# Performance work log

Measured on AMD Instinct MI355X. Metric: run time of the kernel, lower is better.

Reference implementation:

```python
import jax, jax.numpy as jnp
import numpy as np

N_NODES = 100000
N_EDGES = 1600000
IN_CH = 64
HID = 64


def setup_inputs() -> dict:
    key = jax.random.key(0)
    ks = jax.random.split(key, 7)
    x = jax.random.normal(ks[0], (N_NODES, IN_CH), dtype=jnp.float32)
    edge_index = jax.random.randint(ks[1], (2, N_EDGES), 0, N_NODES, dtype=jnp.int64)
    node_pair = jax.random.randint(ks[2], (2,), 0, N_NODES, dtype=jnp.int64)
    W1 = jax.random.normal(ks[3], (IN_CH, HID), dtype=jnp.float32) / np.float32(np.sqrt(IN_CH))
    b1 = jnp.zeros((HID,), dtype=jnp.float32)
    W2 = jax.random.normal(ks[4], (HID, HID), dtype=jnp.float32) / np.float32(np.sqrt(HID))
    b2 = jnp.zeros((HID,), dtype=jnp.float32)
    fc_W = jax.random.normal(ks[5], (2 * HID, 1), dtype=jnp.float32) / np.float32(np.sqrt(2 * HID))
    fc_b = jnp.zeros((1,), dtype=jnp.float32)
    return {"x": x, "edge_index": edge_index, "node_pair": node_pair,
            "W1": W1, "b1": b1, "W2": W2, "b2": b2, "fc_W": fc_W, "fc_b": fc_b}


def gcn_conv(x, W, b, src, dst, n):
    # linear transform then symmetric-normalized scatter-add with self-loops (PyG GCNConv)
    h = x @ W                                   # [n, out]
    loop = jnp.arange(n, dtype=src.dtype)
    s = jnp.concatenate([src, loop])            # [E+n]
    d = jnp.concatenate([dst, loop])
    deg = jax.ops.segment_sum(jnp.ones_like(d, dtype=h.dtype), d, num_segments=n)
    dinv = jnp.where(deg > 0, jax.lax.rsqrt(deg), 0.0)
    norm = dinv[s] * dinv[d]                    # [E+n]
    out = jax.ops.segment_sum(h[s] * norm[:, None], d, num_segments=n)
    return out + b


def reference(x, edge_index, node_pair, W1, b1, W2, b2, fc_W, fc_b):
    src, dst = edge_index[0], edge_index[1]
    n = x.shape[0]
    h = jax.nn.relu(gcn_conv(x, W1, b1, src, dst, n))
    h = jax.nn.relu(gcn_conv(h, W2, b2, src, dst, n))
    z = jnp.concatenate([h[node_pair[0]], h[node_pair[1]]], axis=0)  # [2*HID]
    return jax.nn.sigmoid(z @ fc_W + fc_b)      # [1]
```

## Files before the change

kernel.cpp:

```cpp
#include <hip/hip_runtime.h>
#include <math.h>


#define CH 64
#define E1CAP 4096
#define F1CAP (E1CAP + 2)
#define E2CAP 131072
#define GRID 256
#define BLK 512
#define NWAVE (BLK / 64)
#define NP5 8
#define BMCAP 3200
#define SPIN_MAX (1 << 20)

struct Params {
    const float* x;
    const int* src; const int* dst; const int* np_;
    const float* W1; const float* b1;
    const float* W2; const float* b2;
    const float* fcW; const float* fcb;
    int* bar;
    int* ctrl;
    int* deg;
    unsigned* bmF1; unsigned* bmNd;
    int* pos1; long long* e1sd; int* F1;
    long long* e2sd; float* h1; float* agg1e;
    float* out;
    int E; int N; int bmN;
};

__device__ __forceinline__ float dinv_of(int degv) {
    return rsqrtf((float)(degv + 1));
}

__device__ __forceinline__ void st_agent(int* p, int v) {
    __hip_atomic_store(p, v, __ATOMIC_RELAXED, __HIP_MEMORY_SCOPE_AGENT);
}
__device__ __forceinline__ void st_agent_f(float* p, float v) {
    __hip_atomic_store(p, v, __ATOMIC_RELAXED, __HIP_MEMORY_SCOPE_AGENT);
}
__device__ __forceinline__ void st_agent64(long long* p, long long v) {
    __hip_atomic_store(p, v, __ATOMIC_RELAXED, __HIP_MEMORY_SCOPE_AGENT);
}
__device__ __forceinline__ int ld_agent(const int* p) {
    return __hip_atomic_load((int*)p, __ATOMIC_RELAXED, __HIP_MEMORY_SCOPE_AGENT);
}
__device__ __forceinline__ long long ld_agent64(const long long* p) {
    return __hip_atomic_load((long long*)p, __ATOMIC_RELAXED, __HIP_MEMORY_SCOPE_AGENT);
}
__device__ __forceinline__ float ld_agent_f(const float* p) {
    return __hip_atomic_load((float*)p, __ATOMIC_RELAXED, __HIP_MEMORY_SCOPE_AGENT);
}

__device__ __forceinline__ void gbar_arrive(int* bar, int phase) {
    __syncthreads();
    if (threadIdx.x == 0) {
        asm volatile("" ::: "memory");
        st_agent(&bar[blockIdx.x << 4], phase);
    }
}
__device__ __forceinline__ void gbar_wait(int* bar, int phase) {
    if (threadIdx.x < 64) {
        const int l = threadIdx.x;
        for (int it = 0; ; ++it) {
            int a = ld_agent(&bar[l << 4]);
            int b = ld_agent(&bar[(l + 64) << 4]);
            int c = ld_agent(&bar[(l + 128) << 4]);
            int d = ld_agent(&bar[(l + 192) << 4]);
            if (__all(min(min(a, b), min(c, d)) >= phase) || it > SPIN_MAX) break;
            __builtin_amdgcn_s_sleep(1);
        }
    }
    __syncthreads();
}
__device__ __forceinline__ void gbar(int* bar, int phase) {
    gbar_arrive(bar, phase);
    gbar_wait(bar, phase);
}

__device__ __forceinline__ void reg_node(int u, unsigned* bmF1, unsigned* bmNd,
                                         int* ctrl, int* F1, int* pos1) {
    unsigned bit = 1u << (u & 31);
    unsigned old = atomicOr(&bmF1[u >> 5], bit);
    if (!(old & bit)) {
        atomicOr(&bmNd[u >> 5], bit);
        int i = atomicAdd(&ctrl[2], 1);
        st_agent(&F1[i], u);
        st_agent(&pos1[u], i);
    }
}

__device__ __forceinline__ long long pack_sd(int s, int d) {
    return ((long long)(unsigned)d << 32) | (unsigned)s;
}

__device__ __forceinline__ void phase_e1f1(int gid, int gsz,
                                           const int* __restrict__ src,
                                           const int* __restrict__ dst, int E,
                                           int p0, int p1, int* ctrl,
                                           long long* e1sd,
                                           unsigned* bmF1, unsigned* bmNd,
                                           int* F1, int* pos1) {
    if (gid == 0) {
        reg_node(p0, bmF1, bmNd, ctrl, F1, pos1);
        if (p1 != p0) reg_node(p1, bmF1, bmNd, ctrl, F1, pos1);
    }
    const int nvec = E >> 2;
    const int4* dst4 = (const int4*)dst;
    for (int base = gid; base < nvec; base += gsz * 4) {
        int4 v[4];
#pragma unroll
        for (int t = 0; t < 4; t++) {
            int i = base + t * gsz;
            if (i < nvec) v[t] = dst4[i];
        }
#pragma unroll
        for (int t = 0; t < 4; t++) {
            int i = base + t * gsz;
            if (i >= nvec) continue;
            int ds[4] = {v[t].x, v[t].y, v[t].z, v[t].w};
#pragma unroll
            for (int k = 0; k < 4; k++) {
                int d = ds[k];
                if (d == p0 || d == p1) {
                    int s = src[i * 4 + k];
                    int idx = atomicAdd(&ctrl[0], 1);
                    if (idx < E1CAP) st_agent64(&e1sd[idx], pack_sd(s, d));
                    reg_node(s, bmF1, bmNd, ctrl, F1, pos1);
                }
            }
        }
    }
    for (int e = (nvec << 2) + gid; e < E; e += gsz) {
        int d = dst[e];
        if (d == p0 || d == p1) {
            int s = src[e];
            int idx = atomicAdd(&ctrl[0], 1);
            if (idx < E1CAP) st_agent64(&e1sd[idx], pack_sd(s, d));
            reg_node(s, bmF1, bmNd, ctrl, F1, pos1);
        }
    }
}

__device__ __forceinline__ void phase_e2(int tid, int gid, int gsz,
                                         const int* __restrict__ src,
                                         const int* __restrict__ dst, int E,
                                         const unsigned* __restrict__ bmF1,
                                         unsigned* bmNd, int* ctrl,
                                         long long* e2sd,
                                         unsigned* lbm, int bmN) {
    const bool lds_ok = (bmN <= BMCAP);
    if (lds_ok)
        for (int i = tid; i < bmN; i += BLK) lbm[i] = bmF1[i];
    __syncthreads();
    const int nvec = E >> 2;
    const int4* dst4 = (const int4*)dst;
    for (int base = gid; base < nvec; base += gsz * 4) {
        int4 v[4];
#pragma unroll
        for (int t = 0; t < 4; t++) {
            int i = base + t * gsz;
            if (i < nvec) v[t] = dst4[i];
        }
#pragma unroll
        for (int t = 0; t < 4; t++) {
            int i = base + t * gsz;
            if (i >= nvec) continue;
            int ds[4] = {v[t].x, v[t].y, v[t].z, v[t].w};
#pragma unroll
            for (int k = 0; k < 4; k++) {
                int d = ds[k];
                unsigned word;
                if (lds_ok) word = lbm[d >> 5]; else word = bmF1[d >> 5];
                if ((word >> (d & 31)) & 1u) {
                    int s = src[i * 4 + k];
                    atomicOr(&bmNd[s >> 5], 1u << (s & 31));
                    int idx = atomicAdd(&ctrl[1], 1);
                    if (idx < E2CAP) st_agent64(&e2sd[idx], pack_sd(s, d));
                }
            }
        }
    }
    for (int e = (nvec << 2) + gid; e < E; e += gsz) {
        int d = dst[e];
        unsigned word;
        if (lds_ok) word = lbm[d >> 5]; else word = bmF1[d >> 5];
        if ((word >> (d & 31)) & 1u) {
            int s = src[e];
            atomicOr(&bmNd[s >> 5], 1u << (s & 31));
            int idx = atomicAdd(&ctrl[1], 1);
            if (idx < E2CAP) st_agent64(&e2sd[idx], pack_sd(s, d));
        }
    }
}

__device__ __forceinline__ void phase_deg(int tid, int gid, int gsz,
                                          const int* __restrict__ dst, int E,
                                          const unsigned* __restrict__ bmNd,
                                          int* deg, unsigned* lbm, int bmN) {
    const bool lds_ok = (bmN <= BMCAP);
    if (lds_ok)
        for (int i = tid; i < bmN; i += BLK) lbm[i] = bmNd[i];
    __syncthreads();
    const int nvec = E >> 2;
    const int4* dst4 = (const int4*)dst;
    for (int base = gid; base < nvec; base += gsz * 4) {
        int4 v[4];
#pragma unroll
        for (int t = 0; t < 4; t++) {
            int i = base + t * gsz;
            if (i < nvec) v[t] = dst4[i];
        }
#pragma unroll
        for (int t = 0; t < 4; t++) {
            int i = base + t * gsz;
            if (i >= nvec) continue;
            int ds[4] = {v[t].x, v[t].y, v[t].z, v[t].w};
#pragma unroll
            for (int k = 0; k < 4; k++) {
                int d = ds[k];
                unsigned word;
                if (lds_ok) word = lbm[d >> 5]; else word = bmNd[d >> 5];
                if ((word >> (d & 31)) & 1u) atomicAdd(&deg[d], 1);
            }
        }
    }
    for (int e = (nvec << 2) + gid; e < E; e += gsz) {
        int d = dst[e];
        unsigned word;
        if (lds_ok) word = lbm[d >> 5]; else word = bmNd[d >> 5];
        if ((word >> (d & 31)) & 1u) atomicAdd(&deg[d], 1);
    }
}

__device__ __forceinline__ void phase_agg(int gid, int gsz,
                                          const float* __restrict__ x,
                                          const int* __restrict__ deg,
                                          const int* __restrict__ pos1,
                                          const int* __restrict__ ctrl,
                                          const long long* __restrict__ e2sd,
                                          const int* __restrict__ F1,
                                          float* __restrict__ agg1e) {
    int cnt2 = min(ld_agent(&ctrl[1]), E2CAP);
    int nf1  = min(ld_agent(&ctrl[2]), F1CAP);
    int total = (cnt2 + nf1) << 6;
    for (int idx = gid; idx < total; idx += gsz) {
        int e = idx >> 6, c = idx & 63;
        int row; float val;
        if (e < cnt2) {
            long long sd = ld_agent64(&e2sd[e]);
            int s = (int)(sd & 0xffffffffll), u = (int)(sd >> 32);
            float nrm = dinv_of(ld_agent(&deg[s])) * dinv_of(ld_agent(&deg[u]));
            row = ld_agent(&pos1[u]);
            val = nrm * x[(size_t)s * CH + c];
        } else {
            int i = e - cnt2;
            int u = ld_agent(&F1[i]);
            float du = dinv_of(ld_agent(&deg[u]));
            row = i;
            val = du * du * x[(size_t)u * CH + c];
        }
        atomicAdd(&agg1e[row * CH + c], val);
    }
}

__device__ __forceinline__ void phase_h1g(int blockId, int tid,
                                          const float* __restrict__ W1,
                                          const float* __restrict__ b1,
                                          const int* __restrict__ ctrl,
                                          const float* __restrict__ agg1e,
                                          float* __restrict__ h1,
                                          float (*a)[CH]) {
    int nf1 = min(ld_agent(&ctrl[2]), F1CAP);
    int w = tid >> 6, j = tid & 63;
    for (int i = blockId * NWAVE + w; i < nf1; i += NP5 * NWAVE) {
        a[w][j] = ld_agent_f(&agg1e[i * CH + j]);
        float sum = b1[j];
#pragma unroll
        for (int k = 0; k < CH; k++) sum += a[w][k] * W1[k * CH + j];
        st_agent_f(&h1[i * CH + j], fmaxf(sum, 0.f));
    }
}

__device__ __forceinline__ void phase_tail(int tid,
                                           const float* __restrict__ h1,
                                           const int* __restrict__ deg,
                                           const int* __restrict__ pos1,
                                           const int* __restrict__ np_,
                                           const int* __restrict__ ctrl,
                                           const long long* __restrict__ e1sd,
                                           const float* __restrict__ W2,
                                           const float* __restrict__ b2,
                                           const float* __restrict__ fcW,
                                           const float* __restrict__ fcb,
                                           float* __restrict__ out,
                                           float (*a2p)[CH], float (*a2)[CH],
                                           float* partial) {
    int w = tid >> 6, j = tid & 63;
    int t = w >> 2, sub = w & 3;
    int pp = np_[t];
    float dp = dinv_of(ld_agent(&deg[pp]));
    float acc = (sub == 0)
        ? dp * dp * ld_agent_f(&h1[ld_agent(&pos1[pp]) * CH + j]) : 0.f;
    int cnt1 = min(ld_agent(&ctrl[0]), E1CAP);
    for (int e = sub; e < cnt1; e += 4) {
        long long sd = ld_agent64(&e1sd[e]);
        int s = (int)(sd & 0xffffffffll), d = (int)(sd >> 32);
        if (d == pp) {
            acc += dinv_of(ld_agent(&deg[s])) * dp *
                   ld_agent_f(&h1[ld_agent(&pos1[s]) * CH + j]);
        }
    }
    a2p[w][j] = acc;
    __syncthreads();
    if (tid < 128) {
        int t2 = tid >> 6;
        a2[t2][j] = a2p[t2 * 4][j] + a2p[t2 * 4 + 1][j] +
                    a2p[t2 * 4 + 2][j] + a2p[t2 * 4 + 3][j];
    }
    __syncthreads();
    if (tid < 128) {
        int t2 = tid >> 6;
        float sum = b2[j];
#pragma unroll
        for (int k = 0; k < CH; k++) sum += a2[t2][k] * W2[k * CH + j];
        float v = fmaxf(sum, 0.f);
        float pr = v * fcW[t2 * CH + j];
        for (int off = 32; off > 0; off >>= 1) pr += __shfl_down(pr, off);
        if (j == 0) partial[t2] = pr;
    }
    __syncthreads();
    if (tid == 0) {
        float z = partial[0] + partial[1] + fcb[0];
        out[0] = 1.f / (1.f + expf(-z));
    }
}

__global__ __launch_bounds__(BLK, 1) void k_fused(Params p) {
    __shared__ unsigned lbm[BMCAP];
    __shared__ float a[NWAVE][CH];
    __shared__ float a2p[NWAVE][CH];
    __shared__ float a2[2][CH];
    __shared__ float partial[2];
    const int gid = blockIdx.x * BLK + threadIdx.x;
    const int gsz = GRID * BLK;

    phase_e1f1(gid, gsz, p.src, p.dst, p.E, p.np_[0], p.np_[1], p.ctrl,
               p.e1sd, p.bmF1, p.bmNd, p.F1, p.pos1);
    gbar(p.bar, 1);
    phase_e2(threadIdx.x, gid, gsz, p.src, p.dst, p.E, p.bmF1, p.bmNd,
             p.ctrl, p.e2sd, lbm, p.bmN);
    gbar(p.bar, 2);
    phase_deg(threadIdx.x, gid, gsz, p.dst, p.E, p.bmNd, p.deg, lbm, p.bmN);
    gbar(p.bar, 3);
    phase_agg(gid, gsz, p.x, p.deg, p.pos1, p.ctrl, p.e2sd, p.F1, p.agg1e);
    if (blockIdx.x >= NP5) {
        gbar_arrive(p.bar, 5);
        return;
    }
    gbar(p.bar, 4);
    phase_h1g(blockIdx.x, threadIdx.x, p.W1, p.b1, p.ctrl, p.agg1e, p.h1, a);
    gbar_arrive(p.bar, 5);
    if (blockIdx.x != 0) return;
    gbar_wait(p.bar, 5);
    phase_tail(threadIdx.x, p.h1, p.deg, p.pos1, p.np_, p.ctrl, p.e1sd,
               p.W2, p.b2, p.fcW, p.fcb, (float*)p.out, a2p, a2, partial);
}

extern "C" void kernel_launch(void* const* d_in, const int* in_sizes, int n_in,
                              void* d_out, int out_size, void* d_ws, size_t ws_size,
                              hipStream_t stream) {
    const float* x   = (const float*)d_in[0];
    const int*   ei  = (const int*)d_in[1];
    const int*   np_ = (const int*)d_in[2];

    const int N = in_sizes[0] / CH;
    const int E = in_sizes[1] / 2;
    const int bmN = (N + 31) / 32;

    char* w = (char*)d_ws;
    size_t off = 0;
    auto alloc = [&](size_t bytes) {
        size_t o = off;
        off = (off + bytes + 255) & ~((size_t)255);
        return o;
    };
    size_t o_bar  = alloc((size_t)GRID * 16 * 4);
    size_t o_ctrl = alloc(64);
    size_t o_bmF1 = alloc((size_t)bmN * 4);
    size_t o_bmNd = alloc((size_t)bmN * 4);
    size_t o_deg  = alloc((size_t)N * 4);
    size_t o_agg  = alloc((size_t)F1CAP * CH * 4);
    size_t zero_end = off;
    size_t o_pos  = alloc((size_t)N * 4);
    size_t o_e1sd = alloc((size_t)E1CAP * 8);
    size_t o_F1   = alloc((size_t)F1CAP * 4);
    size_t o_e2sd = alloc((size_t)E2CAP * 8);
    size_t o_h1   = alloc((size_t)F1CAP * CH * 4);
    (void)ws_size;

    Params p;
    p.x    = x;
    p.src  = ei;
    p.dst  = ei + E;
    p.np_  = np_;
    p.W1   = (const float*)d_in[3];
    p.b1   = (const float*)d_in[4];
    p.W2   = (const float*)d_in[5];
    p.b2   = (const float*)d_in[6];
    p.fcW  = (const float*)d_in[7];
    p.fcb  = (const float*)d_in[8];
    p.bar   = (int*)(w + o_bar);
    p.ctrl  = (int*)(w + o_ctrl);
    p.bmF1  = (unsigned*)(w + o_bmF1);
    p.bmNd  = (unsigned*)(w + o_bmNd);
    p.deg   = (int*)(w + o_deg);
    p.agg1e = (float*)(w + o_agg);
    p.pos1  = (int*)(w + o_pos);
    p.e1sd  = (long long*)(w + o_e1sd);
    p.F1    = (int*)(w + o_F1);
    p.e2sd  = (long long*)(w + o_e2sd);
    p.h1    = (float*)(w + o_h1);
    p.out  = (float*)d_out;
    p.E = E; p.N = N; p.bmN = bmN;

    (void)hipMemsetAsync(d_ws, 0, zero_end, stream);

    k_fused<<<GRID, BLK, 0, stream>>>(p);
}
```

Before: 122.2 us.

## Fuse degree counting for frontier nodes into E2 pass and drop a grid barrier

The E2 edge scan now also counts degrees for frontier-1 destinations directly. The later degree pass only handles the remaining source nodes, tracked in a separate bitmap, so that scan does fewer atomics. The h1 transform and the tail computation move into block 0 alone, with h1 kept in LDS when the frontier is small. This removes one grid-wide barrier and the multi-block h1 phase, at the cost of serialising the h1 GEMV work on a single block.

```diff
diff --git a/kernel.cpp b/kernel.cpp
--- a/kernel.cpp
+++ b/kernel.cpp
@@ -9,8 +9,8 @@
 #define GRID 256
 #define BLK 512
 #define NWAVE (BLK / 64)
-#define NP5 8
 #define BMCAP 3200
+#define HCAP 256
 #define SPIN_MAX (1 << 20)
 
 struct Params {
@@ -22,9 +22,9 @@
     int* bar;
     int* ctrl;
     int* deg;
-    unsigned* bmF1; unsigned* bmNd;
+    unsigned* bmF1; unsigned* bmOut;
     int* pos1; long long* e1sd; int* F1;
-    long long* e2sd; float* h1; float* agg1e;
+    long long* e2sd; float* h1g; float* agg1e;
     float* out;
     int E; int N; int bmN;
 };
@@ -44,6 +44,9 @@
 }
 __device__ __forceinline__ int ld_agent(const int* p) {
     return __hip_atomic_load((int*)p, __ATOMIC_RELAXED, __HIP_MEMORY_SCOPE_AGENT);
+}
+__device__ __forceinline__ unsigned ld_agent_u(const unsigned* p) {
+    return __hip_atomic_load((unsigned*)p, __ATOMIC_RELAXED, __HIP_MEMORY_SCOPE_AGENT);
 }
 __device__ __forceinline__ long long ld_agent64(const long long* p) {
     return __hip_atomic_load((long long*)p, __ATOMIC_RELAXED, __HIP_MEMORY_SCOPE_AGENT);
@@ -78,12 +81,11 @@
     gbar_wait(bar, phase);
 }
 
-__device__ __forceinline__ void reg_node(int u, unsigned* bmF1, unsigned* bmNd,
+__device__ __forceinline__ void reg_node(int u, unsigned* bmF1,
                                          int* ctrl, int* F1, int* pos1) {
     unsigned bit = 1u << (u & 31);
     unsigned old = atomicOr(&bmF1[u >> 5], bit);
     if (!(old & bit)) {
-        atomicOr(&bmNd[u >> 5], bit);
         int i = atomicAdd(&ctrl[2], 1);
         st_agent(&F1[i], u);
         st_agent(&pos1[u], i);
@@ -98,12 +100,11 @@
                                            const int* __restrict__ src,
                                            const int* __restrict__ dst, int E,
                                            int p0, int p1, int* ctrl,
-                                           long long* e1sd,
-                                           unsigned* bmF1, unsigned* bmNd,
+                                           long long* e1sd, unsigned* bmF1,
                                            int* F1, int* pos1) {
     if (gid == 0) {
-        reg_node(p0, bmF1, bmNd, ctrl, F1, pos1);
-        if (p1 != p0) reg_node(p1, bmF1, bmNd, ctrl, F1, pos1);
+        reg_node(p0, bmF1, ctrl, F1, pos1);
+        if (p1 != p0) reg_node(p1, bmF1, ctrl, F1, pos1);
     }
     const int nvec = E >> 2;
     const int4* dst4 = (const int4*)dst;
@@ -126,7 +127,7 @@
                     int s = src[i * 4 + k];
                     int idx = atomicAdd(&ctrl[0], 1);
                     if (idx < E1CAP) st_agent64(&e1sd[idx], pack_sd(s, d));
-                    reg_node(s, bmF1, bmNd, ctrl, F1, pos1);
+                    reg_node(s, bmF1, ctrl, F1, pos1);
                 }
             }
         }
@@ -137,21 +138,21 @@
             int s = src[e];
             int idx = atomicAdd(&ctrl[0], 1);
             if (idx < E1CAP) st_agent64(&e1sd[idx], pack_sd(s, d));
-            reg_node(s, bmF1, bmNd, ctrl, F1, pos1);
-        }
-    }
-}
-
-__device__ __forceinline__ void phase_e2(int tid, int gid, int gsz,
-                                         const int* __restrict__ src,
-                                         const int* __restrict__ dst, int E,
-                                         const unsigned* __restrict__ bmF1,
-                                         unsigned* bmNd, int* ctrl,
-                                         long long* e2sd,
-                                         unsigned* lbm, int bmN) {
+            reg_node(s, bmF1, ctrl, F1, pos1);
+        }
+    }
+}
+
+__device__ __forceinline__ void phase_e2deg(int tid, int gid, int gsz,
+                                            const int* __restrict__ src,
+                                            const int* __restrict__ dst, int E,
+                                            const unsigned* __restrict__ bmF1,
+                                            unsigned* bmOut, int* deg,
+                                            int* ctrl, long long* e2sd,
+                                            unsigned* lbm, int bmN) {
     const bool lds_ok = (bmN <= BMCAP);
     if (lds_ok)
-        for (int i = tid; i < bmN; i += BLK) lbm[i] = bmF1[i];
+        for (int i = tid; i < bmN; i += BLK) lbm[i] = ld_agent_u(&bmF1[i]);
     __syncthreads();
     const int nvec = E >> 2;
     const int4* dst4 = (const int4*)dst;
@@ -170,11 +171,13 @@
 #pragma unroll
             for (int k = 0; k < 4; k++) {
                 int d = ds[k];
-                unsigned word;
-                if (lds_ok) word = lbm[d >> 5]; else word = bmF1[d >> 5];
+                unsigned word = lds_ok ? lbm[d >> 5] : ld_agent_u(&bmF1[d >> 5]);
                 if ((word >> (d & 31)) & 1u) {
                     int s = src[i * 4 + k];
-                    atomicOr(&bmNd[s >> 5], 1u << (s & 31));
+                    atomicAdd(&deg[d], 1);
+                    unsigned sw = lds_ok ? lbm[s >> 5] : ld_agent_u(&bmF1[s >> 5]);
+                    if (!((sw >> (s & 31)) & 1u))
+                        atomicOr(&bmOut[s >> 5], 1u << (s & 31));
                     int idx = atomicAdd(&ctrl[1], 1);
                     if (idx < E2CAP) st_agent64(&e2sd[idx], pack_sd(s, d));
                 }
@@ -183,24 +186,27 @@
     }
     for (int e = (nvec << 2) + gid; e < E; e += gsz) {
         int d = dst[e];
-        unsigned word;
-        if (lds_ok) word = lbm[d >> 5]; else word = bmF1[d >> 5];
+        unsigned word = lds_ok ? lbm[d >> 5] : ld_agent_u(&bmF1[d >> 5]);
         if ((word >> (d & 31)) & 1u) {
             int s = src[e];
-            atomicOr(&bmNd[s >> 5], 1u << (s & 31));
+            atomicAdd(&deg[d], 1);
+            unsigned sw = lds_ok ? lbm[s >> 5] : ld_agent_u(&bmF1[s >> 5]);
+            if (!((sw >> (s & 31)) & 1u))
+                atomicOr(&bmOut[s >> 5], 1u << (s & 31));
             int idx = atomicAdd(&ctrl[1], 1);
             if (idx < E2CAP) st_agent64(&e2sd[idx], pack_sd(s, d));
         }
     }
 }
 
-__device__ __forceinline__ void phase_deg(int tid, int gid, int gsz,
-                                          const int* __restrict__ dst, int E,
-                                          const unsigned* __restrict__ bmNd,
-                                          int* deg, unsigned* lbm, int bmN) {
+__device__ __forceinline__ void phase_degout(int tid, int gid, int gsz,
+                                             const int* __restrict__ dst, int E,
+                                             const unsigned* __restrict__ bmOut,
+                                             int* deg, unsigned* lbm, int bmN) {
     const bool lds_ok = (bmN <= BMCAP);
+    __syncthreads();
     if (lds_ok)
-        for (int i = tid; i < bmN; i += BLK) lbm[i] = bmNd[i];
+        for (int i = tid; i < bmN; i += BLK) lbm[i] = ld_agent_u(&bmOut[i]);
     __syncthreads();
     const int nvec = E >> 2;
     const int4* dst4 = (const int4*)dst;
@@ -219,16 +225,14 @@
 #pragma unroll
             for (int k = 0; k < 4; k++) {
                 int d = ds[k];
-                unsigned word;
-                if (lds_ok) word = lbm[d >> 5]; else word = bmNd[d >> 5];
+                unsigned word = lds_ok ? lbm[d >> 5] : ld_agent_u(&bmOut[d >> 5]);
                 if ((word >> (d & 31)) & 1u) atomicAdd(&deg[d], 1);
             }
         }
     }
     for (int e = (nvec << 2) + gid; e < E; e += gsz) {
         int d = dst[e];
-        unsigned word;
-        if (lds_ok) word = lbm[d >> 5]; else word = bmNd[d >> 5];
+        unsigned word = lds_ok ? lbm[d >> 5] : ld_agent_u(&bmOut[d >> 5]);
         if ((word >> (d & 31)) & 1u) atomicAdd(&deg[d], 1);
     }
 }
@@ -264,107 +268,85 @@
     }
 }
 
-__device__ __forceinline__ void phase_h1g(int blockId, int tid,
-                                          const float* __restrict__ W1,
-                                          const float* __restrict__ b1,
-                                          const int* __restrict__ ctrl,
-                                          const float* __restrict__ agg1e,
-                                          float* __restrict__ h1,
-                                          float (*a)[CH]) {
-    int nf1 = min(ld_agent(&ctrl[2]), F1CAP);
-    int w = tid >> 6, j = tid & 63;
-    for (int i = blockId * NWAVE + w; i < nf1; i += NP5 * NWAVE) {
-        a[w][j] = ld_agent_f(&agg1e[i * CH + j]);
-        float sum = b1[j];
-#pragma unroll
-        for (int k = 0; k < CH; k++) sum += a[w][k] * W1[k * CH + j];
-        st_agent_f(&h1[i * CH + j], fmaxf(sum, 0.f));
-    }
-}
-
-__device__ __forceinline__ void phase_tail(int tid,
-                                           const float* __restrict__ h1,
-                                           const int* __restrict__ deg,
-                                           const int* __restrict__ pos1,
-                                           const int* __restrict__ np_,
-                                           const int* __restrict__ ctrl,
-                                           const long long* __restrict__ e1sd,
-                                           const float* __restrict__ W2,
-                                           const float* __restrict__ b2,
-                                           const float* __restrict__ fcW,
-                                           const float* __restrict__ fcb,
-                                           float* __restrict__ out,
-                                           float (*a2p)[CH], float (*a2)[CH],
-                                           float* partial) {
-    int w = tid >> 6, j = tid & 63;
-    int t = w >> 2, sub = w & 3;
-    int pp = np_[t];
-    float dp = dinv_of(ld_agent(&deg[pp]));
-    float acc = (sub == 0)
-        ? dp * dp * ld_agent_f(&h1[ld_agent(&pos1[pp]) * CH + j]) : 0.f;
-    int cnt1 = min(ld_agent(&ctrl[0]), E1CAP);
-    for (int e = sub; e < cnt1; e += 4) {
-        long long sd = ld_agent64(&e1sd[e]);
-        int s = (int)(sd & 0xffffffffll), d = (int)(sd >> 32);
-        if (d == pp) {
-            acc += dinv_of(ld_agent(&deg[s])) * dp *
-                   ld_agent_f(&h1[ld_agent(&pos1[s]) * CH + j]);
-        }
-    }
-    a2p[w][j] = acc;
-    __syncthreads();
-    if (tid < 128) {
-        int t2 = tid >> 6;
-        a2[t2][j] = a2p[t2 * 4][j] + a2p[t2 * 4 + 1][j] +
-                    a2p[t2 * 4 + 2][j] + a2p[t2 * 4 + 3][j];
-    }
-    __syncthreads();
-    if (tid < 128) {
-        int t2 = tid >> 6;
-        float sum = b2[j];
-#pragma unroll
-        for (int k = 0; k < CH; k++) sum += a2[t2][k] * W2[k * CH + j];
-        float v = fmaxf(sum, 0.f);
-        float pr = v * fcW[t2 * CH + j];
-        for (int off = 32; off > 0; off >>= 1) pr += __shfl_down(pr, off);
-        if (j == 0) partial[t2] = pr;
-    }
-    __syncthreads();
-    if (tid == 0) {
-        float z = partial[0] + partial[1] + fcb[0];
-        out[0] = 1.f / (1.f + expf(-z));
-    }
-}
-
 __global__ __launch_bounds__(BLK, 1) void k_fused(Params p) {
     __shared__ unsigned lbm[BMCAP];
+    __shared__ float h1l[HCAP][CH];
     __shared__ float a[NWAVE][CH];
     __shared__ float a2p[NWAVE][CH];
     __shared__ float a2[2][CH];
     __shared__ float partial[2];
     const int gid = blockIdx.x * BLK + threadIdx.x;
     const int gsz = GRID * BLK;
+    const int tid = threadIdx.x;
 
     phase_e1f1(gid, gsz, p.src, p.dst, p.E, p.np_[0], p.np_[1], p.ctrl,
-               p.e1sd, p.bmF1, p.bmNd, p.F1, p.pos1);
+               p.e1sd, p.bmF1, p.F1, p.pos1);
     gbar(p.bar, 1);
-    phase_e2(threadIdx.x, gid, gsz, p.src, p.dst, p.E, p.bmF1, p.bmNd,
-             p.ctrl, p.e2sd, lbm, p.bmN);
+    phase_e2deg(tid, gid, gsz, p.src, p.dst, p.E, p.bmF1, p.bmOut, p.deg,
+                p.ctrl, p.e2sd, lbm, p.bmN);
     gbar(p.bar, 2);
-    phase_deg(threadIdx.x, gid, gsz, p.dst, p.E, p.bmNd, p.deg, lbm, p.bmN);
+    phase_degout(tid, gid, gsz, p.dst, p.E, p.bmOut, p.deg, lbm, p.bmN);
     gbar(p.bar, 3);
     phase_agg(gid, gsz, p.x, p.deg, p.pos1, p.ctrl, p.e2sd, p.F1, p.agg1e);
-    if (blockIdx.x >= NP5) {
-        gbar_arrive(p.bar, 5);
-        return;
-    }
-    gbar(p.bar, 4);
-    phase_h1g(blockIdx.x, threadIdx.x, p.W1, p.b1, p.ctrl, p.agg1e, p.h1, a);
-    gbar_arrive(p.bar, 5);
+    gbar_arrive(p.bar, 4);
     if (blockIdx.x != 0) return;
-    gbar_wait(p.bar, 5);
-    phase_tail(threadIdx.x, p.h1, p.deg, p.pos1, p.np_, p.ctrl, p.e1sd,
-               p.W2, p.b2, p.fcW, p.fcb, (float*)p.out, a2p, a2, partial);
+    gbar_wait(p.bar, 4);
+
+    const int nf1  = min(ld_agent(&p.ctrl[2]), F1CAP);
+    const int cnt1 = min(ld_agent(&p.ctrl[0]), E1CAP);
+    const bool h_lds = (nf1 <= HCAP);
+    const int w = tid >> 6, j = tid & 63;
+    for (int i = w; i < nf1; i += NWAVE) {
+        a[w][j] = ld_agent_f(&p.agg1e[i * CH + j]);
+        float sum = p.b1[j];
+#pragma unroll
+        for (int k = 0; k < CH; k++) sum += a[w][k] * p.W1[k * CH + j];
+        float hv = fmaxf(sum, 0.f);
+        if (h_lds) h1l[i][j] = hv; else p.h1g[i * CH + j] = hv;
+    }
+    __syncthreads();
+
+    {
+        int t = w >> 2, sub = w & 3;
+        int pp = p.np_[t];
+        float dp = dinv_of(ld_agent(&p.deg[pp]));
+        int rp = ld_agent(&p.pos1[pp]);
+        float acc = 0.f;
+        if (sub == 0)
+            acc = dp * dp * (h_lds ? h1l[rp][j] : p.h1g[rp * CH + j]);
+        for (int e = sub; e < cnt1; e += 4) {
+            long long sd = ld_agent64(&p.e1sd[e]);
+            int s = (int)(sd & 0xffffffffll), d = (int)(sd >> 32);
+            if (d == pp) {
+                int rs = ld_agent(&p.pos1[s]);
+                float hv = h_lds ? h1l[rs][j] : p.h1g[rs * CH + j];
+                acc += dinv_of(ld_agent(&p.deg[s])) * dp * hv;
+            }
+        }
+        a2p[w][j] = acc;
+    }
+    __syncthreads();
+    if (tid < 128) {
+        int t2 = tid >> 6;
+        a2[t2][j] = a2p[t2 * 4][j] + a2p[t2 * 4 + 1][j] +
+                    a2p[t2 * 4 + 2][j] + a2p[t2 * 4 + 3][j];
+    }
+    __syncthreads();
+    if (tid < 128) {
+        int t2 = tid >> 6;
+        float sum = p.b2[j];
+#pragma unroll
+        for (int k = 0; k < CH; k++) sum += a2[t2][k] * p.W2[k * CH + j];
+        float v = fmaxf(sum, 0.f);
+        float pr = v * p.fcW[t2 * CH + j];
+        for (int off = 32; off > 0; off >>= 1) pr += __shfl_down(pr, off);
+        if (j == 0) partial[t2] = pr;
+    }
+    __syncthreads();
+    if (tid == 0) {
+        float z = partial[0] + partial[1] + p.fcb[0];
+        ((float*)p.out)[0] = 1.f / (1.f + expf(-z));
+    }
 }
 
 extern "C" void kernel_launch(void* const* d_in, const int* in_sizes, int n_in,
@@ -388,7 +370,7 @@
     size_t o_bar  = alloc((size_t)GRID * 16 * 4);
     size_t o_ctrl = alloc(64);
     size_t o_bmF1 = alloc((size_t)bmN * 4);
-    size_t o_bmNd = alloc((size_t)bmN * 4);
+    size_t o_bmOut= alloc((size_t)bmN * 4);
     size_t o_deg  = alloc((size_t)N * 4);
     size_t o_agg  = alloc((size_t)F1CAP * CH * 4);
     size_t zero_end = off;
@@ -413,14 +395,14 @@
     p.bar   = (int*)(w + o_bar);
     p.ctrl  = (int*)(w + o_ctrl);
     p.bmF1  = (unsigned*)(w + o_bmF1);
-    p.bmNd  = (unsigned*)(w + o_bmNd);
+    p.bmOut = (unsigned*)(w + o_bmOut);
     p.deg   = (int*)(w + o_deg);
     p.agg1e = (float*)(w + o_agg);
     p.pos1  = (int*)(w + o_pos);
     p.e1sd  = (long long*)(w + o_e1sd);
     p.F1    = (int*)(w + o_F1);
     p.e2sd  = (long long*)(w + o_e2sd);
-    p.h1    = (float*)(w + o_h1);
+    p.h1g   = (float*)(w + o_h1);
     p.out  = (float*)d_out;
     p.E = E; p.N = N; p.bmN = bmN;
 
```

New measurement: 123.7 us. About the same (+1.2%).
